# Kernel optimization log

Measured on AMD Instinct MI355X. Metric: run time of the kernel, lower is better.

Reference implementation:

```python
import jax, jax.numpy as jnp
import numpy as np

EMBED_DIM = 1024
NUM_HEADS = 16
HEAD_DIM = EMBED_DIM // NUM_HEADS


def setup_inputs() -> dict:
    key = jax.random.key(0)
    k1, k2, k3, k4, k5 = jax.random.split(key, 5)
    B, N, C = 4, 2048, EMBED_DIM
    s = 1.0 / np.sqrt(C)
    return {
        "x": jax.random.normal(k1, (B, N, C), dtype=jnp.float32),
        "w_qkv": jax.random.uniform(k2, (C, 3 * C), dtype=jnp.float32, minval=-s, maxval=s),
        "b_qkv": jax.random.uniform(k3, (3 * C,), dtype=jnp.float32, minval=-s, maxval=s),
        "w_out": jax.random.uniform(k4, (C, C), dtype=jnp.float32, minval=-s, maxval=s),
        "b_out": jax.random.uniform(k5, (C,), dtype=jnp.float32, minval=-s, maxval=s),
    }


def reference(x, w_qkv, b_qkv, w_out, b_out):
    B, N, C = x.shape
    H, D = NUM_HEADS, HEAD_DIM
    qkv = x @ w_qkv + b_qkv                       # [B, N, 3C]
    qkv = qkv.reshape(B, N, 3, H, D)
    q = qkv[:, :, 0].transpose(0, 2, 1, 3)        # [B, H, N, D]
    k = qkv[:, :, 1].transpose(0, 2, 1, 3)
    v = qkv[:, :, 2].transpose(0, 2, 1, 3)
    scale = 1.0 / np.sqrt(D).astype(np.float32)
    attn = jnp.einsum('bhnd,bhmd->bhnm', q, k) * scale  # [B, H, N, N]
    attn = jax.nn.softmax(attn, axis=-1)
    out = jnp.einsum('bhnm,bhmd->bhnd', attn, v)  # [B, H, N, D]
    out = out.transpose(0, 2, 1, 3).reshape(B, N, C)
    return out @ w_out + b_out
```

## Files before the change

### kernel.cpp

```cpp
#include <hip/hip_runtime.h>


typedef unsigned short u16;
typedef unsigned long long u64;
typedef __bf16 bf16x8 __attribute__((ext_vector_type(8)));
typedef float f32x4 __attribute__((ext_vector_type(4)));
typedef unsigned int u32x2 __attribute__((ext_vector_type(2)));

#define MFMA(a, b, c) __builtin_amdgcn_mfma_f32_16x16x32_bf16(a, b, c, 0, 0, 0)

#define QSCALE 0.18033688011112043f

__device__ __forceinline__ u16 f2bf(float f) {
    __bf16 h = (__bf16)f;
    return *(u16*)&h;
}

__device__ __forceinline__ float fexp2(float x) {
#if __has_builtin(__builtin_amdgcn_exp2f)
    return __builtin_amdgcn_exp2f(x);
#else
    return __expf(x * 0.6931471805599453f);
#endif
}

__device__ __forceinline__ void gld16(const void* g, void* l) {
    __builtin_amdgcn_global_load_lds(
        (const __attribute__((address_space(1))) void*)g,
        (__attribute__((address_space(3))) void*)l, 16, 0, 0);
}

__global__ __launch_bounds__(256) void cvt_f32_bf16(
    const float* __restrict__ src, u16* __restrict__ dst, long n)
{
    long i = ((long)blockIdx.x * 256 + threadIdx.x) * 8;
    if (i >= n) return;
    float4 a = *(const float4*)&src[i];
    float4 b = *(const float4*)&src[i + 4];
    union { u16 u[8]; uint4 v; } tmp;
    tmp.u[0] = f2bf(a.x); tmp.u[1] = f2bf(a.y);
    tmp.u[2] = f2bf(a.z); tmp.u[3] = f2bf(a.w);
    tmp.u[4] = f2bf(b.x); tmp.u[5] = f2bf(b.y);
    tmp.u[6] = f2bf(b.z); tmp.u[7] = f2bf(b.w);
    *(uint4*)&dst[i] = tmp.v;
}

__global__ __launch_bounds__(256) void transpose_f2b(
    const float* __restrict__ src, u16* __restrict__ dst, int R, int C)
{
    __shared__ alignas(16) u16 tile[64 * 80];
    const int r0 = blockIdx.y * 64, c0 = blockIdx.x * 64;
    const int t = threadIdx.x;
#pragma unroll
    for (int c = 0; c < 4; c++) {
        int idx = t + c * 256;
        int r = idx >> 4, seg = idx & 15;
        float4 f = *(const float4*)&src[(long)(r0 + r) * C + c0 + seg * 4];
        u16* p = &tile[r * 80 + seg * 4];
        p[0] = f2bf(f.x); p[1] = f2bf(f.y); p[2] = f2bf(f.z); p[3] = f2bf(f.w);
    }
    __syncthreads();
#pragma unroll
    for (int c = 0; c < 2; c++) {
        int idx = t + c * 256;
        int rr = idx >> 3, seg = idx & 7;
        union { u16 u[8]; uint4 v; } tmp;
#pragma unroll
        for (int j = 0; j < 8; j++) tmp.u[j] = tile[(seg * 8 + j) * 80 + rr];
        *(uint4*)&dst[(long)(c0 + rr) * R + r0 + seg * 8] = tmp.v;
    }
}

template <int EPI>
__global__ __launch_bounds__(256) void gemm_bf16(
    const u16* __restrict__ A, const u16* __restrict__ Bt,
    const float* __restrict__ bias,
    u16* __restrict__ out0, u16* __restrict__ out1, u16* __restrict__ out2,
    float* __restrict__ outf,
    int M, int N, int K)
{
    const int m0 = blockIdx.x * 128, n0 = blockIdx.y * 128;
    const int t = threadIdx.x;
    const int wave = t >> 6, lane = t & 63, quad = lane >> 4, l15 = lane & 15;
    const int wm = wave >> 1, wn = wave & 1;

    __shared__ alignas(16) u16 As[128 * 64];
    __shared__ alignas(16) u16 Bs[128 * 64];

    const int srow = wave * 32 + (lane >> 3);
    const int scol = (((lane & 7) ^ (lane >> 3)) & 7) * 8;

    f32x4 acc[4][4] = {};

    for (int k0 = 0; k0 < K; k0 += 64) {
        __syncthreads();
#pragma unroll
        for (int c = 0; c < 4; c++) {
            gld16(&A[(long)(m0 + srow + c * 8) * K + k0 + scol],
                  &As[(wave * 32 + c * 8) * 64]);
            gld16(&Bt[(long)(n0 + srow + c * 8) * K + k0 + scol],
                  &Bs[(wave * 32 + c * 8) * 64]);
        }
        __syncthreads();

#pragma unroll
        for (int ks = 0; ks < 2; ks++) {
            bf16x8 af[4], bf[4];
#pragma unroll
            for (int mt = 0; mt < 4; mt++) {
                int row = wm * 64 + mt * 16 + l15;
                af[mt] = *(bf16x8*)&As[row * 64 + (((ks * 4 + quad) ^ (row & 7)) * 8)];
            }
#pragma unroll
            for (int nt = 0; nt < 4; nt++) {
                int row = wn * 64 + nt * 16 + l15;
                bf[nt] = *(bf16x8*)&Bs[row * 64 + (((ks * 4 + quad) ^ (row & 7)) * 8)];
            }
#pragma unroll
            for (int mt = 0; mt < 4; mt++)
#pragma unroll
                for (int nt = 0; nt < 4; nt++)
                    acc[mt][nt] = MFMA(bf[nt], af[mt], acc[mt][nt]);
        }
    }

#pragma unroll
    for (int mt = 0; mt < 4; mt++) {
        int token = m0 + wm * 64 + mt * 16 + l15;
        int bb = token >> 11, nn = token & 2047;
#pragma unroll
        for (int nt = 0; nt < 4; nt++) {
            int cgb = n0 + wn * 64 + nt * 16 + quad * 4;
            float4 bv = *(const float4*)&bias[cgb];
            float v0 = acc[mt][nt][0] + bv.x;
            float v1 = acc[mt][nt][1] + bv.y;
            float v2 = acc[mt][nt][2] + bv.z;
            float v3 = acc[mt][nt][3] + bv.w;
            if (EPI == 0) {
                int t3 = cgb >> 10;
                int hh = (cgb >> 6) & 15, dd = cgb & 63;
                int bh = (bb << 4) + hh;
                if (t3 == 0) {
                    union { u16 u[4]; u64 v; } pk;
                    pk.u[0] = f2bf(v0 * QSCALE); pk.u[1] = f2bf(v1 * QSCALE);
                    pk.u[2] = f2bf(v2 * QSCALE); pk.u[3] = f2bf(v3 * QSCALE);
                    *(u64*)&out0[((long)bh * 2048 + nn) * 64 + dd] = pk.v;
                } else if (t3 == 1) {
                    union { u16 u[4]; u64 v; } pk;
                    pk.u[0] = f2bf(v0); pk.u[1] = f2bf(v1);
                    pk.u[2] = f2bf(v2); pk.u[3] = f2bf(v3);
                    *(u64*)&out1[((long)bh * 2048 + nn) * 64 + dd] = pk.v;
                } else {
                    long vbo = ((long)bh * 64 + dd) * 2048 + nn;
                    out2[vbo]            = f2bf(v0);
                    out2[vbo + 2048]     = f2bf(v1);
                    out2[vbo + 2 * 2048] = f2bf(v2);
                    out2[vbo + 3 * 2048] = f2bf(v3);
                }
            } else {
                float4 o4 = { v0, v1, v2, v3 };
                *(float4*)&outf[(long)token * N + cgb] = o4;
            }
        }
    }
}

__global__ __launch_bounds__(256, 2) void flash_attn(
    const u16* __restrict__ q, const u16* __restrict__ k,
    const u16* __restrict__ vt, u16* __restrict__ attn)
{
    const int bh = blockIdx.x;
    const int b = bh >> 4, h = bh & 15;
    const int q0 = blockIdx.y * 256;
    const int t = threadIdx.x;
    const int wave = t >> 6, lane = t & 63, quad = lane >> 4, l15 = lane & 15;

    __shared__ alignas(16) u16 Ks[2][4096];
    __shared__ alignas(16) u16 Vs[2][4096];

    const u16* kb = k + (long)bh * 2048 * 64;
    const u16* vb = vt + (long)bh * 64 * 2048;

    bf16x8 qf[4][2];
#pragma unroll
    for (int mt = 0; mt < 4; mt++) {
        long row = (long)bh * 2048 + q0 + wave * 64 + mt * 16 + l15;
        qf[mt][0] = *(const bf16x8*)&q[row * 64 + quad * 8];
        qf[mt][1] = *(const bf16x8*)&q[row * 64 + 32 + quad * 8];
    }

    bf16x8 ones;
#pragma unroll
    for (int j = 0; j < 8; j++) ones[j] = (__bf16)1.0f;

    const int ri = lane >> 3;
    const int ci = (lane & 7) ^ ri;
    const int sg = wave * 2;

    const int lperm = (l15 & 3) | ((l15 & 4) << 1) | ((l15 & 8) >> 1);
    const int swk = (quad ^ (lperm & 7)) * 8;
    const int swv = (quad ^ (l15 & 7)) * 8;

    const int koff0 = lperm * 64 + swk;
    const int koff1 = lperm * 64 + (swk ^ 32);
    const int voff0 = l15 * 64 + swv;
    const int voff1 = l15 * 64 + (swv ^ 32);

    f32x4 o[4][4] = {};
    f32x4 ls[4] = {};

    const u16* kp0 = kb + (long)((sg + 0) * 8 + ri) * 64 + ci * 8;
    const u16* kp1 = kb + (long)((sg + 1) * 8 + ri) * 64 + ci * 8;
    const u16* vp0 = vb + (long)((sg + 0) * 8 + ri) * 2048 + ci * 8;
    const u16* vp1 = vb + (long)((sg + 1) * 8 + ri) * 2048 + ci * 8;

    gld16(kp0, &Ks[0][(sg + 0) * 512]);
    gld16(kp1, &Ks[0][(sg + 1) * 512]);
    gld16(vp0, &Vs[0][(sg + 0) * 512]);
    gld16(vp1, &Vs[0][(sg + 1) * 512]);
    kp0 += 4096; kp1 += 4096; vp0 += 64; vp1 += 64;

    for (int kt2 = 0; kt2 < 16; kt2++) {
#pragma unroll
        for (int half = 0; half < 2; half++) {
            const int cur = half;
            const bool stage_next = (half == 0) | (kt2 < 15);

            __syncthreads();

            if (stage_next) {
                gld16(kp0, &Ks[cur ^ 1][(sg + 0) * 512]);
                gld16(kp1, &Ks[cur ^ 1][(sg + 1) * 512]);
                gld16(vp0, &Vs[cur ^ 1][(sg + 0) * 512]);
                gld16(vp1, &Vs[cur ^ 1][(sg + 1) * 512]);
                kp0 += 4096; kp1 += 4096; vp0 += 64; vp1 += 64;
            }

            bf16x8 pb[4][2];
#pragma unroll
            for (int hp = 0; hp < 2; hp++) {
                f32x4 st[4][2];
                __builtin_amdgcn_s_setprio(1);
#pragma unroll
                for (int c = 0; c < 2; c++) {
                    const int ct = hp * 2 + c;
                    bf16x8 kf0 = *(const bf16x8*)&Ks[cur][ct * 1024 + koff0];
                    bf16x8 kf1 = *(const bf16x8*)&Ks[cur][ct * 1024 + koff1];
#pragma unroll
                    for (int mt = 0; mt < 4; mt++) {
                        f32x4 z = {};
                        z = MFMA(kf0, qf[mt][0], z);
                        st[mt][c] = MFMA(kf1, qf[mt][1], z);
                    }
                }
                __builtin_amdgcn_s_setprio(0);
#pragma unroll
                for (int mt = 0; mt < 4; mt++) {
                    unsigned w[2][2];
#pragma unroll
                    for (int c = 0; c < 2; c++)
#pragma unroll
                        for (int p = 0; p < 2; p++) {
                            u16 lo = f2bf(fexp2(st[mt][c][2 * p]));
                            u16 hi = f2bf(fexp2(st[mt][c][2 * p + 1]));
                            w[c][p] = (unsigned)lo | ((unsigned)hi << 16);
                        }
                    u32x2 pa0 = __builtin_amdgcn_permlane32_swap(
                        w[0][0], w[1][0], false, false);
                    u32x2 pa1 = __builtin_amdgcn_permlane32_swap(
                        w[0][1], w[1][1], false, false);
                    union { unsigned d[4]; bf16x8 v; } uu;
                    uu.d[0] = pa0[0];
                    uu.d[1] = pa1[0];
                    uu.d[2] = pa0[1];
                    uu.d[3] = pa1[1];
                    pb[mt][hp] = uu.v;
                }
            }

#pragma unroll
            for (int mt = 0; mt < 4; mt++) {
                ls[mt] = MFMA(ones, pb[mt][0], ls[mt]);
                ls[mt] = MFMA(ones, pb[mt][1], ls[mt]);
            }

            __builtin_amdgcn_s_setprio(1);
#pragma unroll
            for (int dt = 0; dt < 4; dt++) {
                bf16x8 va0 = *(const bf16x8*)&Vs[cur][dt * 1024 + voff0];
                bf16x8 va1 = *(const bf16x8*)&Vs[cur][dt * 1024 + voff1];
#pragma unroll
                for (int mt = 0; mt < 4; mt++) {
                    o[mt][dt] = MFMA(va0, pb[mt][0], o[mt][dt]);
                    o[mt][dt] = MFMA(va1, pb[mt][1], o[mt][dt]);
                }
            }
            __builtin_amdgcn_s_setprio(0);
        }
    }

#pragma unroll
    for (int mt = 0; mt < 4; mt++) {
        float inv = 1.f / ls[mt][0];
        int n = q0 + wave * 64 + mt * 16 + l15;
#pragma unroll
        for (int dt = 0; dt < 4; dt++) {
            union { u16 u[4]; u64 v; } pk;
#pragma unroll
            for (int r = 0; r < 4; r++) pk.u[r] = f2bf(o[mt][dt][r] * inv);
            *(u64*)&attn[((long)b * 2048 + n) * 1024 + h * 64 + dt * 16 + quad * 4] =
                pk.v;
        }
    }
}

extern "C" void kernel_launch(void* const* d_in, const int* in_sizes, int n_in,
                              void* d_out, int out_size, void* d_ws, size_t ws_size,
                              hipStream_t stream) {
    const float* x     = (const float*)d_in[0];
    const float* w_qkv = (const float*)d_in[1];
    const float* b_qkv = (const float*)d_in[2];
    const float* w_out = (const float*)d_in[3];
    const float* b_out = (const float*)d_in[4];
    float* out = (float*)d_out;

    u16* ws    = (u16*)d_ws;
    u16* q     = ws;
    u16* kk    = q + 8388608;
    u16* vt    = kk + 8388608;
    u16* attn  = vt + 8388608;
    u16* x_bf  = attn + 8388608;
    u16* wqkvT = x_bf + 8388608;
    u16* woutT = wqkvT + 3145728;

    cvt_f32_bf16<<<4096, 256, 0, stream>>>(x, x_bf, 8388608L);
    transpose_f2b<<<dim3(48, 16), 256, 0, stream>>>(w_qkv, wqkvT, 1024, 3072);
    transpose_f2b<<<dim3(16, 16), 256, 0, stream>>>(w_out, woutT, 1024, 1024);
    gemm_bf16<0><<<dim3(64, 24), 256, 0, stream>>>(x_bf, wqkvT, b_qkv, q, kk, vt,
                                                   nullptr, 8192, 3072, 1024);
    flash_attn<<<dim3(64, 8), 256, 0, stream>>>(q, kk, vt, attn);
    gemm_bf16<1><<<dim3(64, 8), 256, 0, stream>>>(attn, woutT, b_out, nullptr,
                                                  nullptr, nullptr, out,
                                                  8192, 1024, 1024);
}
```

Before: 277.0 us.

## Load K/V fragments directly from global into registers, dropping LDS staging

Removes the double-buffered shared-memory staging of K and V tiles and the per-tile block barriers in the attention kernel. Each wave now loads its MFMA K and V fragments straight from global memory into registers, prefetching the next tile while the current one is computed. This removes synchronisation and LDS traffic, but each wave fetches the full K/V stream on its own (four times the global/L2 traffic per block), adds register pressure, and exposes global-load latency. The last prefetch also reads slightly past the current head's data.

```diff
diff --git a/kernel.cpp b/kernel.cpp
--- a/kernel.cpp
+++ b/kernel.cpp
@@ -175,9 +175,6 @@
     const int t = threadIdx.x;
     const int wave = t >> 6, lane = t & 63, quad = lane >> 4, l15 = lane & 15;
 
-    __shared__ alignas(16) u16 Ks[2][4096];
-    __shared__ alignas(16) u16 Vs[2][4096];
-
     const u16* kb = k + (long)bh * 2048 * 64;
     const u16* vb = vt + (long)bh * 64 * 2048;
 
@@ -193,110 +190,96 @@
 #pragma unroll
     for (int j = 0; j < 8; j++) ones[j] = (__bf16)1.0f;
 
-    const int ri = lane >> 3;
-    const int ci = (lane & 7) ^ ri;
-    const int sg = wave * 2;
-
     const int lperm = (l15 & 3) | ((l15 & 4) << 1) | ((l15 & 8) >> 1);
-    const int swk = (quad ^ (lperm & 7)) * 8;
-    const int swv = (quad ^ (l15 & 7)) * 8;
-
-    const int koff0 = lperm * 64 + swk;
-    const int koff1 = lperm * 64 + (swk ^ 32);
-    const int voff0 = l15 * 64 + swv;
-    const int voff1 = l15 * 64 + (swv ^ 32);
+
+    const u16* kp = kb + lperm * 64 + quad * 8;
+    const u16* vp = vb + (long)l15 * 2048 + quad * 8;
+
+    bf16x8 kfr[4][2], vfr[4][2];
+#pragma unroll
+    for (int ct = 0; ct < 4; ct++) {
+        kfr[ct][0] = *(const bf16x8*)&kp[ct * 1024];
+        kfr[ct][1] = *(const bf16x8*)&kp[ct * 1024 + 32];
+    }
+#pragma unroll
+    for (int dt = 0; dt < 4; dt++) {
+        vfr[dt][0] = *(const bf16x8*)&vp[(long)dt * 32768];
+        vfr[dt][1] = *(const bf16x8*)&vp[(long)dt * 32768 + 32];
+    }
 
     f32x4 o[4][4] = {};
     f32x4 ls[4] = {};
 
-    const u16* kp0 = kb + (long)((sg + 0) * 8 + ri) * 64 + ci * 8;
-    const u16* kp1 = kb + (long)((sg + 1) * 8 + ri) * 64 + ci * 8;
-    const u16* vp0 = vb + (long)((sg + 0) * 8 + ri) * 2048 + ci * 8;
-    const u16* vp1 = vb + (long)((sg + 1) * 8 + ri) * 2048 + ci * 8;
-
-    gld16(kp0, &Ks[0][(sg + 0) * 512]);
-    gld16(kp1, &Ks[0][(sg + 1) * 512]);
-    gld16(vp0, &Vs[0][(sg + 0) * 512]);
-    gld16(vp1, &Vs[0][(sg + 1) * 512]);
-    kp0 += 4096; kp1 += 4096; vp0 += 64; vp1 += 64;
-
-    for (int kt2 = 0; kt2 < 16; kt2++) {
-#pragma unroll
-        for (int half = 0; half < 2; half++) {
-            const int cur = half;
-            const bool stage_next = (half == 0) | (kt2 < 15);
-
-            __syncthreads();
-
-            if (stage_next) {
-                gld16(kp0, &Ks[cur ^ 1][(sg + 0) * 512]);
-                gld16(kp1, &Ks[cur ^ 1][(sg + 1) * 512]);
-                gld16(vp0, &Vs[cur ^ 1][(sg + 0) * 512]);
-                gld16(vp1, &Vs[cur ^ 1][(sg + 1) * 512]);
-                kp0 += 4096; kp1 += 4096; vp0 += 64; vp1 += 64;
-            }
-
-            bf16x8 pb[4][2];
-#pragma unroll
-            for (int hp = 0; hp < 2; hp++) {
-                f32x4 st[4][2];
-                __builtin_amdgcn_s_setprio(1);
-#pragma unroll
-                for (int c = 0; c < 2; c++) {
-                    const int ct = hp * 2 + c;
-                    bf16x8 kf0 = *(const bf16x8*)&Ks[cur][ct * 1024 + koff0];
-                    bf16x8 kf1 = *(const bf16x8*)&Ks[cur][ct * 1024 + koff1];
-#pragma unroll
-                    for (int mt = 0; mt < 4; mt++) {
-                        f32x4 z = {};
-                        z = MFMA(kf0, qf[mt][0], z);
-                        st[mt][c] = MFMA(kf1, qf[mt][1], z);
+    for (int kt = 0; kt < 32; kt++) {
+#pragma unroll
+        for (int hp = 0; hp < 2; hp++) {
+            f32x4 st[4][2];
+            __builtin_amdgcn_s_setprio(1);
+#pragma unroll
+            for (int c = 0; c < 2; c++) {
+                const int ct = hp * 2 + c;
+#pragma unroll
+                for (int mt = 0; mt < 4; mt++) {
+                    f32x4 z = {};
+                    z = MFMA(kfr[ct][0], qf[mt][0], z);
+                    st[mt][c] = MFMA(kfr[ct][1], qf[mt][1], z);
+                }
+            }
+            __builtin_amdgcn_s_setprio(0);
+
+            if (hp == 1) {
+                kp += 4096;
+#pragma unroll
+                for (int ct = 0; ct < 4; ct++) {
+                    kfr[ct][0] = *(const bf16x8*)&kp[ct * 1024];
+                    kfr[ct][1] = *(const bf16x8*)&kp[ct * 1024 + 32];
+                }
+            }
+
+            bf16x8 pb[4];
+#pragma unroll
+            for (int mt = 0; mt < 4; mt++) {
+                unsigned w[2][2];
+#pragma unroll
+                for (int c = 0; c < 2; c++)
+#pragma unroll
+                    for (int p = 0; p < 2; p++) {
+                        u16 lo = f2bf(fexp2(st[mt][c][2 * p]));
+                        u16 hi = f2bf(fexp2(st[mt][c][2 * p + 1]));
+                        w[c][p] = (unsigned)lo | ((unsigned)hi << 16);
                     }
-                }
-                __builtin_amdgcn_s_setprio(0);
-#pragma unroll
-                for (int mt = 0; mt < 4; mt++) {
-                    unsigned w[2][2];
-#pragma unroll
-                    for (int c = 0; c < 2; c++)
-#pragma unroll
-                        for (int p = 0; p < 2; p++) {
-                            u16 lo = f2bf(fexp2(st[mt][c][2 * p]));
-                            u16 hi = f2bf(fexp2(st[mt][c][2 * p + 1]));
-                            w[c][p] = (unsigned)lo | ((unsigned)hi << 16);
-                        }
-                    u32x2 pa0 = __builtin_amdgcn_permlane32_swap(
-                        w[0][0], w[1][0], false, false);
-                    u32x2 pa1 = __builtin_amdgcn_permlane32_swap(
-                        w[0][1], w[1][1], false, false);
-                    union { unsigned d[4]; bf16x8 v; } uu;
-                    uu.d[0] = pa0[0];
-                    uu.d[1] = pa1[0];
-                    uu.d[2] = pa0[1];
-                    uu.d[3] = pa1[1];
-                    pb[mt][hp] = uu.v;
-                }
-            }
-
-#pragma unroll
-            for (int mt = 0; mt < 4; mt++) {
-                ls[mt] = MFMA(ones, pb[mt][0], ls[mt]);
-                ls[mt] = MFMA(ones, pb[mt][1], ls[mt]);
-            }
+                u32x2 pa0 = __builtin_amdgcn_permlane32_swap(
+                    w[0][0], w[1][0], false, false);
+                u32x2 pa1 = __builtin_amdgcn_permlane32_swap(
+                    w[0][1], w[1][1], false, false);
+                union { unsigned d[4]; bf16x8 v; } uu;
+                uu.d[0] = pa0[0];
+                uu.d[1] = pa1[0];
+                uu.d[2] = pa0[1];
+                uu.d[3] = pa1[1];
+                pb[mt] = uu.v;
+            }
+
+#pragma unroll
+            for (int mt = 0; mt < 4; mt++)
+                ls[mt] = MFMA(ones, pb[mt], ls[mt]);
 
             __builtin_amdgcn_s_setprio(1);
 #pragma unroll
-            for (int dt = 0; dt < 4; dt++) {
-                bf16x8 va0 = *(const bf16x8*)&Vs[cur][dt * 1024 + voff0];
-                bf16x8 va1 = *(const bf16x8*)&Vs[cur][dt * 1024 + voff1];
-#pragma unroll
-                for (int mt = 0; mt < 4; mt++) {
-                    o[mt][dt] = MFMA(va0, pb[mt][0], o[mt][dt]);
-                    o[mt][dt] = MFMA(va1, pb[mt][1], o[mt][dt]);
-                }
-            }
+            for (int dt = 0; dt < 4; dt++)
+#pragma unroll
+                for (int mt = 0; mt < 4; mt++)
+                    o[mt][dt] = MFMA(vfr[dt][hp], pb[mt], o[mt][dt]);
             __builtin_amdgcn_s_setprio(0);
-        }
+
+            {
+                const u16* vpn = vp + 64 + hp * 32;
+#pragma unroll
+                for (int dt = 0; dt < 4; dt++)
+                    vfr[dt][hp] = *(const bf16x8*)&vpn[(long)dt * 32768];
+            }
+        }
+        vp += 64;
     }
 
 #pragma unroll
```

Result: slower. 302.3 us (+9.1%).
